# Kernel optimization log

Hardware: AMD Instinct MI355X
Metric: run time of the kernel (lower is better)

## Reference

```python
import jax, jax.numpy as jnp
import numpy as np

EPS = 1e-12  # matches torch F.normalize eps


def setup_inputs() -> dict:
    key = jax.random.key(0)
    k_x, k_w, k_b, k_c, k_f = jax.random.split(key, 5)
    N, C, H, W = 32, 128, 64, 64
    K = 64
    x = jax.random.normal(k_x, (N, C, H, W), dtype=jnp.float32)
    conv_w = jax.random.normal(k_w, (K, C), dtype=jnp.float32) * 0.05  # 1x1 conv weight [K,C,1,1] squeezed
    conv_b = jax.random.normal(k_b, (K,), dtype=jnp.float32) * 0.05
    centroids = jax.random.uniform(k_c, (K, C), dtype=jnp.float32)
    fc_w = jax.random.normal(k_f, (1, K), dtype=jnp.float32) * 0.1  # nn.Linear(K,1,bias=False).weight
    return {"x": x, "conv_w": conv_w, "conv_b": conv_b, "centroids": centroids, "fc_w": fc_w}


def _l2norm(v, axis):
    return v / jnp.maximum(jnp.linalg.norm(v, axis=axis, keepdims=True), EPS)


def reference(x, conv_w, conv_b, centroids, fc_w):
    N, C, H, W = x.shape
    K = conv_w.shape[0]
    # descriptor-wise L2 normalize over channel dim
    x = _l2norm(x, axis=1)
    xf = x.reshape(N, C, H * W)                                   # [N,C,S]
    # 1x1 conv == per-pixel linear over channels
    logits = jnp.einsum('kc,ncs->nks', conv_w, xf) + conv_b[None, :, None]
    a = jax.nn.softmax(logits, axis=1)                            # [N,K,S] soft assignment
    # VLAD: sum_s a[n,k,s] * (x[n,:,s] - centroids[k,:]), loop-free
    vlad = jnp.einsum('nks,ncs->nkc', a, xf) \
           - a.sum(axis=-1)[..., None] * centroids[None, :, :]    # [N,K,C]
    # intra-normalization over descriptor dim
    vlad = _l2norm(vlad, axis=2)
    # lastfc: [N,C,K] @ [K] -> [N,C]
    out = jnp.einsum('nkc,k->nc', vlad, fc_w[0])
    return out
```

## Files before the change

### kernel.cpp

```cpp
#include <hip/hip_runtime.h>
#include <math.h>

#define Nn 32
#define Cc 128
#define Ss 4096
#define Kk 64
#define NCHUNK 16
#define SCHUNK (Ss / NCHUNK)
#define ST 64
#define NSUB (SCHUNK / ST)
#define BLK 256

#define XCS 72
#define XTS 136
#define AS  72
#define RSS 68

typedef __attribute__((ext_vector_type(8))) short short8;
typedef __attribute__((ext_vector_type(4))) float float4v;

__device__ __forceinline__ unsigned f2bf(float f) {
    unsigned u = __builtin_bit_cast(unsigned, f);
    return (u + 0x7fffu + ((u >> 16) & 1u)) >> 16;
}
__device__ __forceinline__ unsigned pack2(float a, float b) {
    return f2bf(a) | (f2bf(b) << 16);
}

__global__ __launch_bounds__(BLK, 2) void netvlad_main(
    const float* __restrict__ x,
    const float* __restrict__ conv_w,
    const float* __restrict__ conv_b,
    float* __restrict__ vlad,
    float* __restrict__ asum)
{
    __shared__ __align__(16) unsigned short xC[Cc * XCS];
    __shared__ __align__(16) unsigned short xT[ST * XTS];
    __shared__ __align__(16) unsigned short aB[Kk * AS];
    __shared__ __align__(16) float red[16 * RSS];
    __shared__ float bias_lds[Kk];
    float* asumLDS = red;

    const int t    = threadIdx.x;
    const int n    = blockIdx.y;
    const int w    = t >> 6;
    const int m    = t & 15;
    const int quad = (t >> 4) & 3;
    const int sw   = 16 * w + m;

    if (t < Kk) bias_lds[t] = conv_b[t];

    short8 wfrag[4][4];
#pragma unroll
    for (int kt = 0; kt < 4; ++kt) {
        const float* wr_ = conv_w + (16 * kt + m) * Cc;
#pragma unroll
        for (int ks = 0; ks < 4; ++ks) {
            float4 wa = *(const float4*)(wr_ + 32 * ks + 8 * quad);
            float4 wb = *(const float4*)(wr_ + 32 * ks + 8 * quad + 4);
            union { short8 s8; unsigned u[4]; } W_;
            W_.u[0] = pack2(wa.x, wa.y);
            W_.u[1] = pack2(wa.z, wa.w);
            W_.u[2] = pack2(wb.x, wb.y);
            W_.u[3] = pack2(wb.z, wb.w);
            wfrag[kt][ks] = W_.s8;
        }
    }

    float4v acc[8];
#pragma unroll
    for (int nt = 0; nt < 8; ++nt) acc[nt] = (float4v){0.f, 0.f, 0.f, 0.f};
    float asum_part[16];
#pragma unroll
    for (int j = 0; j < 16; ++j) asum_part[j] = 0.f;

    const float* xn = x + (size_t)n * Cc * Ss;

    for (int sub = 0; sub < NSUB; ++sub) {
        const int s0 = blockIdx.x * SCHUNK + sub * ST;
        __syncthreads();

        {
            const int g  = t >> 4;
            const int sq = (t & 15) << 2;
            float sp0 = 0.f, sp1 = 0.f, sp2 = 0.f, sp3 = 0.f;
#pragma unroll
            for (int r = 0; r < 8; ++r) {
                int c = g + 16 * r;
                float4 v = *(const float4*)(xn + (size_t)c * Ss + s0 + sq);
                sp0 += v.x * v.x; sp1 += v.y * v.y;
                sp2 += v.z * v.z; sp3 += v.w * v.w;
                uint2 pk = make_uint2(pack2(v.x, v.y), pack2(v.z, v.w));
                *(uint2*)&xC[c * XCS + sq] = pk;
            }
            *(float4*)&red[g * RSS + sq] = make_float4(sp0, sp1, sp2, sp3);
        }
        __syncthreads();

#pragma unroll
        for (int pass = 0; pass < 2; ++pass) {
            int oct = (t >> 5) + 8 * pass;
            int sp2_ = t & 31;
            unsigned r_[8];
#pragma unroll
            for (int j = 0; j < 8; ++j)
                r_[j] = *(const unsigned*)&xC[(8 * oct + j) * XCS + 2 * sp2_];
            uint4 lo, hi;
            lo.x = (r_[0] & 0xffffu) | (r_[1] << 16);
            lo.y = (r_[2] & 0xffffu) | (r_[3] << 16);
            lo.z = (r_[4] & 0xffffu) | (r_[5] << 16);
            lo.w = (r_[6] & 0xffffu) | (r_[7] << 16);
            hi.x = (r_[0] >> 16) | (r_[1] & 0xffff0000u);
            hi.y = (r_[2] >> 16) | (r_[3] & 0xffff0000u);
            hi.z = (r_[4] >> 16) | (r_[5] & 0xffff0000u);
            hi.w = (r_[6] >> 16) | (r_[7] & 0xffff0000u);
            *(uint4*)&xT[(2 * sp2_ + 0) * XTS + 8 * oct] = lo;
            *(uint4*)&xT[(2 * sp2_ + 1) * XTS + 8 * oct] = hi;
        }

        float pr = red[(4 * quad + 0) * RSS + sw] + red[(4 * quad + 1) * RSS + sw]
                 + red[(4 * quad + 2) * RSS + sw] + red[(4 * quad + 3) * RSS + sw];
        pr += __shfl_xor(pr, 16);
        pr += __shfl_xor(pr, 32);
        float invn = 1.0f / fmaxf(sqrtf(pr), 1e-12f);
        __syncthreads();

        float4v Lr[4];
#pragma unroll
        for (int kt = 0; kt < 4; ++kt) Lr[kt] = (float4v){0.f, 0.f, 0.f, 0.f};
#pragma unroll
        for (int ks = 0; ks < 4; ++ks) {
            short8 b = *(const short8*)&xT[sw * XTS + 32 * ks + 8 * quad];
#pragma unroll
            for (int kt = 0; kt < 4; ++kt)
                Lr[kt] = __builtin_amdgcn_mfma_f32_16x16x32_bf16(wfrag[kt][ks], b, Lr[kt], 0, 0, 0);
        }

        {
            float lg[16];
#pragma unroll
            for (int kt = 0; kt < 4; ++kt) {
                lg[4 * kt + 0] = Lr[kt].x * invn + bias_lds[16 * kt + 4 * quad + 0];
                lg[4 * kt + 1] = Lr[kt].y * invn + bias_lds[16 * kt + 4 * quad + 1];
                lg[4 * kt + 2] = Lr[kt].z * invn + bias_lds[16 * kt + 4 * quad + 2];
                lg[4 * kt + 3] = Lr[kt].w * invn + bias_lds[16 * kt + 4 * quad + 3];
            }
            float mx = lg[0];
#pragma unroll
            for (int j = 1; j < 16; ++j) mx = fmaxf(mx, lg[j]);
            mx = fmaxf(mx, __shfl_xor(mx, 16));
            mx = fmaxf(mx, __shfl_xor(mx, 32));
            float lsum = 0.f;
#pragma unroll
            for (int j = 0; j < 16; ++j) { lg[j] = __expf(lg[j] - mx); lsum += lg[j]; }
            lsum += __shfl_xor(lsum, 16);
            lsum += __shfl_xor(lsum, 32);
            float itot = 1.0f / lsum;
            float sca  = itot * invn;
#pragma unroll
            for (int j = 0; j < 16; ++j) asum_part[j] += lg[j] * itot;
#pragma unroll
            for (int kt = 0; kt < 4; ++kt) {
                aB[(16 * kt + 4 * quad + 0) * AS + sw] = (unsigned short)f2bf(lg[4 * kt + 0] * sca);
                aB[(16 * kt + 4 * quad + 1) * AS + sw] = (unsigned short)f2bf(lg[4 * kt + 1] * sca);
                aB[(16 * kt + 4 * quad + 2) * AS + sw] = (unsigned short)f2bf(lg[4 * kt + 2] * sca);
                aB[(16 * kt + 4 * quad + 3) * AS + sw] = (unsigned short)f2bf(lg[4 * kt + 3] * sca);
            }
        }
        __syncthreads();

#pragma unroll
        for (int ks = 0; ks < 2; ++ks) {
            short8 af = *(const short8*)&aB[(16 * w + m) * AS + 32 * ks + 8 * quad];
#pragma unroll
            for (int nt = 0; nt < 8; ++nt) {
                short8 bf_ = *(const short8*)&xC[(16 * nt + m) * XCS + 32 * ks + 8 * quad];
                acc[nt] = __builtin_amdgcn_mfma_f32_16x16x32_bf16(af, bf_, acc[nt], 0, 0, 0);
            }
        }
    }

    float* vb = vlad + ((size_t)n * Kk + 16 * w + 4 * quad) * Cc + m;
#pragma unroll
    for (int nt = 0; nt < 8; ++nt) {
        atomicAdd(vb + 0 * Cc + 16 * nt, acc[nt].x);
        atomicAdd(vb + 1 * Cc + 16 * nt, acc[nt].y);
        atomicAdd(vb + 2 * Cc + 16 * nt, acc[nt].z);
        atomicAdd(vb + 3 * Cc + 16 * nt, acc[nt].w);
    }

#pragma unroll
    for (int j = 0; j < 16; ++j) {
        float v = asum_part[j];
        v += __shfl_xor(v, 1);
        v += __shfl_xor(v, 2);
        v += __shfl_xor(v, 4);
        v += __shfl_xor(v, 8);
        asum_part[j] = v;
    }
    __syncthreads();
    if (m == 0) {
#pragma unroll
        for (int kt = 0; kt < 4; ++kt)
#pragma unroll
            for (int r = 0; r < 4; ++r)
                asumLDS[w * 64 + 16 * kt + 4 * quad + r] = asum_part[4 * kt + r];
    }
    __syncthreads();
    if (t < Kk) {
        float s_ = asumLDS[t] + asumLDS[64 + t] + asumLDS[128 + t] + asumLDS[192 + t];
        atomicAdd(&asum[n * Kk + t], s_);
    }
}

__global__ __launch_bounds__(256) void netvlad_final(
    const float* __restrict__ vlad, const float* __restrict__ asum,
    const float* __restrict__ centroids, const float* __restrict__ fc_w,
    float* __restrict__ out)
{
    __shared__ float scale_s[Kk];
    __shared__ float asum_s[Kk];
    __shared__ float red2[Kk][4];

    const int n = blockIdx.x;
    const int t = threadIdx.x;
    const int k = t >> 2;
    const int q = t & 3;

    const float* vr = vlad + ((size_t)n * Kk + k) * Cc + q * 32;
    const float* cr = centroids + k * Cc + q * 32;
    const float  as = asum[n * Kk + k];

    float ssq = 0.f;
#pragma unroll
    for (int i = 0; i < 8; ++i) {
        float4 v4 = *(const float4*)(vr + 4 * i);
        float4 c4 = *(const float4*)(cr + 4 * i);
        float d0 = v4.x - as * c4.x;
        float d1 = v4.y - as * c4.y;
        float d2 = v4.z - as * c4.z;
        float d3 = v4.w - as * c4.w;
        ssq += d0 * d0 + d1 * d1 + d2 * d2 + d3 * d3;
    }
    red2[k][q] = ssq;
    __syncthreads();
    if (q == 0) {
        float tot = red2[k][0] + red2[k][1] + red2[k][2] + red2[k][3];
        scale_s[k] = fc_w[k] / fmaxf(sqrtf(tot), 1e-12f);
        asum_s[k]  = as;
    }
    __syncthreads();

    if (t < Cc) {
        const int c = t;
        const float* vbp = vlad + (size_t)n * Kk * Cc + c;
        float o = 0.f;
#pragma unroll 8
        for (int k2 = 0; k2 < Kk; ++k2)
            o += scale_s[k2] * (vbp[k2 * Cc] - asum_s[k2] * centroids[k2 * Cc + c]);
        out[n * Cc + c] = o;
    }
}

extern "C" void kernel_launch(void* const* d_in, const int* in_sizes, int n_in,
                              void* d_out, int out_size, void* d_ws, size_t ws_size,
                              hipStream_t stream) {
    (void)in_sizes; (void)n_in; (void)out_size; (void)ws_size;
    const float* x         = (const float*)d_in[0];
    const float* conv_w    = (const float*)d_in[1];
    const float* conv_b    = (const float*)d_in[2];
    const float* centroids = (const float*)d_in[3];
    const float* fc_w      = (const float*)d_in[4];
    float* out = (float*)d_out;

    float* vlad = (float*)d_ws;
    float* asum = vlad + (size_t)Nn * Kk * Cc;
    size_t zero_bytes = ((size_t)Nn * Kk * Cc + (size_t)Nn * Kk) * sizeof(float);
    hipMemsetAsync(d_ws, 0, zero_bytes, stream);

    dim3 grid(NCHUNK, Nn);
    netvlad_main<<<grid, BLK, 0, stream>>>(x, conv_w, conv_b, vlad, asum);
    netvlad_final<<<Nn, 256, 0, stream>>>(vlad, asum, centroids, fc_w, out);
}
```

Baseline: 124.6 us.

## Prefetch next x sub-tile into registers and replace atomics with partial buffers

```diff
diff --git a/kernel.cpp b/kernel.cpp
--- a/kernel.cpp
+++ b/kernel.cpp
@@ -31,8 +31,8 @@
     const float* __restrict__ x,
     const float* __restrict__ conv_w,
     const float* __restrict__ conv_b,
-    float* __restrict__ vlad,
-    float* __restrict__ asum)
+    float* __restrict__ vlad_part,
+    float* __restrict__ asum_part_g)
 {
     __shared__ __align__(16) unsigned short xC[Cc * XCS];
     __shared__ __align__(16) unsigned short xT[ST * XTS];
@@ -74,26 +74,37 @@
 #pragma unroll
     for (int j = 0; j < 16; ++j) asum_part[j] = 0.f;
 
-    const float* xn = x + (size_t)n * Cc * Ss;
-
+    const float* xn  = x + (size_t)n * Cc * Ss;
+    const int g      = t >> 4;
+    const int sq     = (t & 15) << 2;
+    const int sbase  = blockIdx.x * SCHUNK;
+
+    float4 pv[8];
+#pragma unroll
+    for (int r = 0; r < 8; ++r)
+        pv[r] = *(const float4*)(xn + (size_t)(g + 16 * r) * Ss + sbase + sq);
+
+#pragma unroll 1
     for (int sub = 0; sub < NSUB; ++sub) {
-        const int s0 = blockIdx.x * SCHUNK + sub * ST;
         __syncthreads();
 
         {
-            const int g  = t >> 4;
-            const int sq = (t & 15) << 2;
             float sp0 = 0.f, sp1 = 0.f, sp2 = 0.f, sp3 = 0.f;
 #pragma unroll
             for (int r = 0; r < 8; ++r) {
-                int c = g + 16 * r;
-                float4 v = *(const float4*)(xn + (size_t)c * Ss + s0 + sq);
+                float4 v = pv[r];
                 sp0 += v.x * v.x; sp1 += v.y * v.y;
                 sp2 += v.z * v.z; sp3 += v.w * v.w;
                 uint2 pk = make_uint2(pack2(v.x, v.y), pack2(v.z, v.w));
-                *(uint2*)&xC[c * XCS + sq] = pk;
+                *(uint2*)&xC[(g + 16 * r) * XCS + sq] = pk;
             }
             *(float4*)&red[g * RSS + sq] = make_float4(sp0, sp1, sp2, sp3);
+        }
+        if (sub + 1 < NSUB) {
+            const int s0n = sbase + (sub + 1) * ST;
+#pragma unroll
+            for (int r = 0; r < 8; ++r)
+                pv[r] = *(const float4*)(xn + (size_t)(g + 16 * r) * Ss + s0n + sq);
         }
         __syncthreads();
 
@@ -180,13 +191,13 @@
         }
     }
 
-    float* vb = vlad + ((size_t)n * Kk + 16 * w + 4 * quad) * Cc + m;
+    float* vb = vlad_part + (((size_t)blockIdx.x * Nn + n) * Kk + 16 * w + 4 * quad) * Cc + m;
 #pragma unroll
     for (int nt = 0; nt < 8; ++nt) {
-        atomicAdd(vb + 0 * Cc + 16 * nt, acc[nt].x);
-        atomicAdd(vb + 1 * Cc + 16 * nt, acc[nt].y);
-        atomicAdd(vb + 2 * Cc + 16 * nt, acc[nt].z);
-        atomicAdd(vb + 3 * Cc + 16 * nt, acc[nt].w);
+        vb[0 * Cc + 16 * nt] = acc[nt].x;
+        vb[1 * Cc + 16 * nt] = acc[nt].y;
+        vb[2 * Cc + 16 * nt] = acc[nt].z;
+        vb[3 * Cc + 16 * nt] = acc[nt].w;
     }
 
 #pragma unroll
@@ -209,15 +220,16 @@
     __syncthreads();
     if (t < Kk) {
         float s_ = asumLDS[t] + asumLDS[64 + t] + asumLDS[128 + t] + asumLDS[192 + t];
-        atomicAdd(&asum[n * Kk + t], s_);
+        asum_part_g[((size_t)blockIdx.x * Nn + n) * Kk + t] = s_;
     }
 }
 
 __global__ __launch_bounds__(256) void netvlad_final(
-    const float* __restrict__ vlad, const float* __restrict__ asum,
+    const float* __restrict__ vlad_part, const float* __restrict__ asum_part_g,
     const float* __restrict__ centroids, const float* __restrict__ fc_w,
     float* __restrict__ out)
 {
+    __shared__ __align__(16) float vred[Kk * Cc];
     __shared__ float scale_s[Kk];
     __shared__ float asum_s[Kk];
     __shared__ float red2[Kk][4];
@@ -227,38 +239,55 @@
     const int k = t >> 2;
     const int q = t & 3;
 
-    const float* vr = vlad + ((size_t)n * Kk + k) * Cc + q * 32;
+    if (t < Kk) {
+        float s_ = 0.f;
+#pragma unroll
+        for (int ch = 0; ch < NCHUNK; ++ch)
+            s_ += asum_part_g[((size_t)ch * Nn + n) * Kk + t];
+        asum_s[t] = s_;
+    }
+
+    float4 v[8];
+#pragma unroll
+    for (int i = 0; i < 8; ++i) v[i] = make_float4(0.f, 0.f, 0.f, 0.f);
+#pragma unroll 2
+    for (int ch = 0; ch < NCHUNK; ++ch) {
+        const float* base = vlad_part + (((size_t)ch * Nn + n) * Kk + k) * Cc + q * 32;
+#pragma unroll
+        for (int i = 0; i < 8; ++i) {
+            float4 u = *(const float4*)(base + 4 * i);
+            v[i].x += u.x; v[i].y += u.y; v[i].z += u.z; v[i].w += u.w;
+        }
+    }
+    __syncthreads();
+    const float as = asum_s[k];
     const float* cr = centroids + k * Cc + q * 32;
-    const float  as = asum[n * Kk + k];
-
     float ssq = 0.f;
 #pragma unroll
     for (int i = 0; i < 8; ++i) {
-        float4 v4 = *(const float4*)(vr + 4 * i);
         float4 c4 = *(const float4*)(cr + 4 * i);
-        float d0 = v4.x - as * c4.x;
-        float d1 = v4.y - as * c4.y;
-        float d2 = v4.z - as * c4.z;
-        float d3 = v4.w - as * c4.w;
-        ssq += d0 * d0 + d1 * d1 + d2 * d2 + d3 * d3;
+        float4 d;
+        d.x = v[i].x - as * c4.x;
+        d.y = v[i].y - as * c4.y;
+        d.z = v[i].z - as * c4.z;
+        d.w = v[i].w - as * c4.w;
+        ssq += d.x * d.x + d.y * d.y + d.z * d.z + d.w * d.w;
+        *(float4*)&vred[k * Cc + q * 32 + 4 * i] = d;
     }
     red2[k][q] = ssq;
     __syncthreads();
     if (q == 0) {
         float tot = red2[k][0] + red2[k][1] + red2[k][2] + red2[k][3];
         scale_s[k] = fc_w[k] / fmaxf(sqrtf(tot), 1e-12f);
-        asum_s[k]  = as;
     }
     __syncthreads();
 
     if (t < Cc) {
-        const int c = t;
-        const float* vbp = vlad + (size_t)n * Kk * Cc + c;
         float o = 0.f;
 #pragma unroll 8
         for (int k2 = 0; k2 < Kk; ++k2)
-            o += scale_s[k2] * (vbp[k2 * Cc] - asum_s[k2] * centroids[k2 * Cc + c]);
-        out[n * Cc + c] = o;
+            o += scale_s[k2] * vred[k2 * Cc + t];
+        out[n * Cc + t] = o;
     }
 }
 
@@ -273,12 +302,10 @@
     const float* fc_w      = (const float*)d_in[4];
     float* out = (float*)d_out;
 
-    float* vlad = (float*)d_ws;
-    float* asum = vlad + (size_t)Nn * Kk * Cc;
-    size_t zero_bytes = ((size_t)Nn * Kk * Cc + (size_t)Nn * Kk) * sizeof(float);
-    hipMemsetAsync(d_ws, 0, zero_bytes, stream);
+    float* vlad_part = (float*)d_ws;
+    float* asum_part = vlad_part + (size_t)NCHUNK * Nn * Kk * Cc;
 
     dim3 grid(NCHUNK, Nn);
-    netvlad_main<<<grid, BLK, 0, stream>>>(x, conv_w, conv_b, vlad, asum);
-    netvlad_final<<<Nn, 256, 0, stream>>>(vlad, asum, centroids, fc_w, out);
-}
+    netvlad_main<<<grid, BLK, 0, stream>>>(x, conv_w, conv_b, vlad_part, asum_part);
+    netvlad_final<<<Nn, 256, 0, stream>>>(vlad_part, asum_part, centroids, fc_w, out);
+}
```

Measured after the change: 129.1 us. 1.04x slower.
